# Kernel optimization log

Measured on AMD Instinct MI355X. Metric: run time of the kernel, lower is better.

Reference implementation:

```python
import jax, jax.numpy as jnp
import numpy as np

B, LT, LI, D, H, K = 32, 512, 576, 768, 8, 512


def setup_inputs() -> dict:
    key = jax.random.key(0)
    ks = jax.random.split(key, 10)
    s = 0.02
    return {
        "text_hidden_states": jax.random.normal(ks[0], (B, LT, D), jnp.float32),
        "image_hidden_states": jax.random.normal(ks[1], (B, LI, D), jnp.float32),
        "text_mask": jnp.ones((B, LT), jnp.int32),
        "Wb": jax.random.normal(ks[2], (H, D, D), jnp.float32) * s,   # per-head Linear weights [out,in]
        "Wv": jax.random.normal(ks[3], (K, D), jnp.float32) * s,
        "Wq": jax.random.normal(ks[4], (K, D), jnp.float32) * s,
        "Whv": jax.random.normal(ks[5], (K,), jnp.float32) * s,
        "Whq": jax.random.normal(ks[6], (K,), jnp.float32) * s,
        "Wo": jax.random.normal(ks[7], (D, D * H), jnp.float32) * s,  # output_proj weight [out,in]
        "bo": jnp.zeros((D,), jnp.float32),
    }


def reference(text_hidden_states, image_hidden_states, text_mask, Wb, Wv, Wq, Whv, Whq, Wo, bo):
    text, image = text_hidden_states, image_hidden_states
    # per-head text projection (torch Linear: x @ W.T), batched over heads
    pt = jnp.einsum('bxe,hfe->hbxf', text, Wb)                 # [H,B,LT,D]
    aff = jnp.einsum('hbxe,bye->hbxy', pt, image)              # [H,B,LT,LI]
    wv_v = jnp.einsum('bye,ke->byk', image, Wv)                # [B,LI,K] (head-shared)
    wq_q = jnp.einsum('bxe,ke->bxk', text, Wq)                 # [B,LT,K]
    wqqc = jnp.einsum('bxk,hbxy->hbyk', wq_q, aff)             # [H,B,LI,K]
    wvvc = jnp.einsum('byk,hbxy->hbxk', wv_v, aff)             # [H,B,LT,K]
    h_v = jnp.tanh(wv_v[None] + wqqc)
    h_q = jnp.tanh(wq_q[None] + wvvc)
    att_v = jax.nn.softmax(jnp.einsum('hbyk,k->hby', h_v, Whv), axis=-1)  # over image tokens
    att_q = jax.nn.softmax(jnp.einsum('hbxk,k->hbx', h_q, Whq), axis=-1)  # over text tokens
    ctx_v = jnp.einsum('hby,byd->hbd', att_v, image)
    ctx_q = jnp.einsum('hbx,bxd->hbd', att_q, text)
    head_out = ctx_v + ctx_q                                   # [H,B,D]
    combined = jnp.transpose(head_out, (1, 0, 2)).reshape(text.shape[0], -1)  # [B,H*D]
    return combined @ Wo.T + bo
```

## Files before the change

kernel.cpp:

```cpp
#include <hip/hip_runtime.h>
#include <math.h>

#define B_  32
#define LT_ 512
#define LI_ 576
#define LIP 640
#define D_  768
#define H_  8
#define K_  512
#define NTOK  (LI_ + LT_)
#define CSPLIT 8
#define TPB   (NTOK / CSPLIT)
#define NHEAD ((long)H_ * B_ * D_)

typedef __attribute__((ext_vector_type(4))) short short4v;
typedef __attribute__((ext_vector_type(8))) unsigned short ushort8;
typedef __attribute__((ext_vector_type(8))) _Float16 f16x8;
typedef __attribute__((ext_vector_type(4))) float f32x4;

__device__ __forceinline__ unsigned short f2h(float x) {
  _Float16 h = (_Float16)x;
  return __builtin_bit_cast(unsigned short, h);
}
__device__ __forceinline__ float h2f(unsigned short u) {
  return (float)__builtin_bit_cast(_Float16, u);
}
__device__ __forceinline__ float ftanh(float x) {
  float e = __expf(2.f * x);
  return 1.f - 2.f * __builtin_amdgcn_rcpf(e + 1.f);
}

__device__ __forceinline__ void gl_lds16(const void* g, void* l) {
  __builtin_amdgcn_global_load_lds(
      (const __attribute__((address_space(1))) void*)g,
      (__attribute__((address_space(3))) void*)l, 16, 0, 0);
}

#define EPI_PLAIN 0
#define EPI_T     1
#define EPI_TANH  2
#define EPI_OUT   3

struct Seg {
  const unsigned short *A, *B;
  unsigned short *C, *CT;
  const unsigned short* base;
  const float* wvec;
  float* outv;
  long sA, sB, sC, sCT, sBase;
  int Kd, lda, ldb;
  int gx, gy, nblk, epi, Mlim, valid, ldc, ldt;
};
struct Params { Seg s0, s1, s2; };

__global__ __launch_bounds__(256, 2) void mfma_seg(Params p)
{
  const int orig = blockIdx.x, nwg = gridDim.x;
  const int q8 = nwg >> 3, r8 = nwg & 7;
  const int xcd = orig & 7, idx = orig >> 3;
  const int wg = (xcd < r8 ? xcd * (q8 + 1) : r8 * (q8 + 1) + (xcd - r8) * q8) + idx;

  Seg sg; int local;
  if (wg < p.s0.nblk)                      { sg = p.s0; local = wg; }
  else if (wg < p.s0.nblk + p.s1.nblk)     { sg = p.s1; local = wg - p.s0.nblk; }
  else                                     { sg = p.s2; local = wg - p.s0.nblk - p.s1.nblk; }

  const int bx = local % sg.gx;
  const int tmp2 = local / sg.gx;
  const int by = tmp2 % sg.gy, bz = tmp2 / sg.gy;

  __shared__ unsigned short LDSU[24576];
  unsigned short* As = LDSU;
  unsigned short* Bs = LDSU + 16384;

  const int t = threadIdx.x, lane = t & 63, w = t >> 6;
  const int wr = w >> 1, wc = w & 1;
  const int m0 = bx * 256, n0 = by * 128;
  const int Kd = sg.Kd, lda = sg.lda, ldb = sg.ldb, ldc = sg.ldc;
  const unsigned short* A  = sg.A + (long)bz * sg.sA;
  const unsigned short* Bm = sg.B + (long)bz * sg.sB;

  const int rowb = w * 8 + (lane >> 3);
  const int cswz = ((lane & 7) ^ (rowb & 7)) * 8;
  const bool clampA = (m0 + 256 > sg.Mlim);
  const unsigned short* aSrc = A  + (long)(m0 + rowb) * lda + cswz;
  const unsigned short* bSrc = Bm + (long)(n0 + rowb) * ldb + cswz;
  unsigned short* aDst = As + rowb * 64;
  unsigned short* bDst = Bs + rowb * 64;

  f32x4 acc[8][4];
  #pragma unroll
  for (int i = 0; i < 8; ++i)
    #pragma unroll
    for (int j = 0; j < 4; ++j)
      acc[i][j] = (f32x4){0.f, 0.f, 0.f, 0.f};

  const int rl = lane & 15, g = lane >> 4;

  for (int k0 = 0; k0 < Kd; k0 += 64) {
    __syncthreads();
    if (!clampA) {
      #pragma unroll
      for (int q = 0; q < 8; ++q)
        gl_lds16(aSrc + (long)q * 32 * lda + k0, aDst + q * 2048);
    } else {
      #pragma unroll
      for (int q = 0; q < 8; ++q) {
        int rgl = m0 + q * 32 + rowb;
        if (rgl >= sg.Mlim) rgl = sg.Mlim - 1;
        gl_lds16(A + (long)rgl * lda + cswz + k0, aDst + q * 2048);
      }
    }
    #pragma unroll
    for (int q = 0; q < 4; ++q)
      gl_lds16(bSrc + (long)q * 32 * ldb + k0, bDst + q * 2048);
    __syncthreads();

    #pragma unroll
    for (int h2 = 0; h2 < 2; ++h2) {
      const int slot = (((h2 << 2) | g) ^ (rl & 7)) << 3;
      f16x8 af[8], bf[4];
      #pragma unroll
      for (int i = 0; i < 8; ++i)
        af[i] = *(const f16x8*)&As[(wr * 128 + i * 16 + rl) * 64 + slot];
      #pragma unroll
      for (int j = 0; j < 4; ++j)
        bf[j] = *(const f16x8*)&Bs[(wc * 64 + j * 16 + rl) * 64 + slot];
      #pragma unroll
      for (int i = 0; i < 8; ++i)
        #pragma unroll
        for (int j = 0; j < 4; ++j)
          acc[i][j] = __builtin_amdgcn_mfma_f32_16x16x32_f16(af[i], bf[j], acc[i][j], 0, 0, 0);
    }
  }

  const int rg = lane >> 4;
  if (sg.epi <= EPI_T) {
    unsigned short* C = sg.C + (long)bz * sg.sC;
    #pragma unroll
    for (int i = 0; i < 8; ++i)
      #pragma unroll
      for (int j = 0; j < 4; ++j)
        #pragma unroll
        for (int rr = 0; rr < 4; ++rr) {
          int ml = wr * 128 + i * 16 + rg * 4 + rr;
          int nl = wc * 64 + j * 16 + rl;
          if (m0 + ml < sg.Mlim)
            C[(long)(m0 + ml) * ldc + n0 + nl] = f2h(acc[i][j][rr]);
        }
    if (sg.epi == EPI_T) {
      unsigned short* CT = sg.CT + (long)bz * sg.sCT;
      __syncthreads();
      #pragma unroll
      for (int pp = 0; pp < 2; ++pp) {
        if (wr == pp) {
          #pragma unroll
          for (int i = 0; i < 8; ++i)
            #pragma unroll
            for (int j = 0; j < 4; ++j) {
              int nl = wc * 64 + j * 16 + rl;
              int mh = i * 16 + rg * 4;
              *(short4v*)&LDSU[nl * 136 + mh] = (short4v){
                  (short)f2h(acc[i][j][0]), (short)f2h(acc[i][j][1]),
                  (short)f2h(acc[i][j][2]), (short)f2h(acc[i][j][3])};
            }
        }
        __syncthreads();
        #pragma unroll
        for (int rr = 0; rr < 8; ++rr) {
          int rn = rr * 16 + (t >> 4);
          int m8 = (t & 15) * 8;
          int mg = m0 + pp * 128 + m8;
          if (mg < sg.Mlim)
            *(ushort8*)(CT + (long)(n0 + rn) * sg.ldt + mg) =
                *(const ushort8*)&LDSU[rn * 136 + m8];
        }
        __syncthreads();
      }
    }
  } else if (sg.epi == EPI_TANH) {
    const unsigned short* base = sg.base + (long)bz * sg.sBase;
    float* outp = sg.outv + (long)bz * sg.valid;
    #pragma unroll
    for (int i = 0; i < 8; ++i)
      #pragma unroll
      for (int rr = 0; rr < 4; ++rr) {
        int row = m0 + wr * 128 + i * 16 + rg * 4 + rr;
        if (row < sg.Mlim) {
          float s = 0.f;
          #pragma unroll
          for (int j = 0; j < 4; ++j) {
            int col = n0 + wc * 64 + j * 16 + rl;
            float v = acc[i][j][rr] + h2f(base[(long)row * ldc + col]);
            s += ftanh(v) * sg.wvec[col];
          }
          s += __shfl_xor(s, 1, 64);
          s += __shfl_xor(s, 2, 64);
          s += __shfl_xor(s, 4, 64);
          s += __shfl_xor(s, 8, 64);
          if (rl == 0 && row < sg.valid)
            atomicAdd(&outp[row], s);
        }
      }
  } else {
    float* outp = sg.outv;
    if (wr == 0) {
      #pragma unroll
      for (int i = 0; i < 2; ++i)
        #pragma unroll
        for (int rr = 0; rr < 4; ++rr) {
          int row = i * 16 + rg * 4 + rr;
          #pragma unroll
          for (int j = 0; j < 4; ++j) {
            int col = n0 + wc * 64 + j * 16 + rl;
            atomicAdd(&outp[(long)row * ldc + col], acc[i][j][rr]);
          }
        }
    }
  }
}

struct CSeg { const float* src; unsigned short* dst; long n8; };

__global__ __launch_bounds__(256) void cast_multi(
    CSeg c0, CSeg c1, CSeg c2, CSeg c3, CSeg c4)
{
  long i = (long)blockIdx.x * 256 + threadIdx.x;
  const float* src; unsigned short* dst;
  if      (i < c0.n8)                 { src = c0.src; dst = c0.dst; }
  else if ((i -= c0.n8) < c1.n8)      { src = c1.src; dst = c1.dst; }
  else if ((i -= c1.n8) < c2.n8)      { src = c2.src; dst = c2.dst; }
  else if ((i -= c2.n8) < c3.n8)      { src = c3.src; dst = c3.dst; }
  else if ((i -= c3.n8) < c4.n8)      { src = c4.src; dst = c4.dst; }
  else return;
  float4 v0 = ((const float4*)src)[i * 2];
  float4 v1 = ((const float4*)src)[i * 2 + 1];
  ushort8 o;
  o[0] = f2h(v0.x); o[1] = f2h(v0.y); o[2] = f2h(v0.z); o[3] = f2h(v0.w);
  o[4] = f2h(v1.x); o[5] = f2h(v1.y); o[6] = f2h(v1.z); o[7] = f2h(v1.w);
  *(ushort8*)(dst + i * 8) = o;
}

__global__ __launch_bounds__(256) void cast_pad_image(
    const float* __restrict__ in, unsigned short* __restrict__ out)
{
  long tid = (long)blockIdx.x * 256 + threadIdx.x;
  const long tot = (long)B_ * LIP * (D_ / 8);
  if (tid >= tot) return;
  int e8 = (int)(tid % (D_ / 8));
  long rw = tid / (D_ / 8);
  int y  = (int)(rw % LIP);
  long b = rw / LIP;
  ushort8 o;
  if (y < LI_) {
    const float* p = in + ((b * LI_ + y) * D_ + e8 * 8);
    float4 v0 = *(const float4*)p, v1 = *(const float4*)(p + 4);
    o[0] = f2h(v0.x); o[1] = f2h(v0.y); o[2] = f2h(v0.z); o[3] = f2h(v0.w);
    o[4] = f2h(v1.x); o[5] = f2h(v1.y); o[6] = f2h(v1.z); o[7] = f2h(v1.w);
  } else {
    #pragma unroll
    for (int j = 0; j < 8; ++j) o[j] = 0;
  }
  *(ushort8*)(out + rw * D_ + e8 * 8) = o;
}

__global__ __launch_bounds__(256) void zero_f32(float* __restrict__ p, long n) {
  long i = (long)blockIdx.x * 256 + threadIdx.x;
  if (i < n) p[i] = 0.f;
}

__global__ __launch_bounds__(256) void init_out(
    const float* __restrict__ bo, float* __restrict__ out)
{
  int i = blockIdx.x * 256 + threadIdx.x;
  out[i] = bo[i % D_];
}

__global__ __launch_bounds__(256) void softmax_att(
    const float* __restrict__ lv, const float* __restrict__ lq,
    float* __restrict__ attvG, float* __restrict__ attqG)
{
  const int b = blockIdx.x, h = blockIdx.y;
  const int t = threadIdx.x;
  __shared__ float buf[LI_];
  __shared__ float red[4];

  const float* lvp = lv + ((long)h * B_ + b) * LI_;
  float m = -1e30f;
  for (int i = t; i < LI_; i += 256) m = fmaxf(m, lvp[i]);
  #pragma unroll
  for (int o = 32; o > 0; o >>= 1) m = fmaxf(m, __shfl_down(m, o, 64));
  if ((t & 63) == 0) red[t >> 6] = m;
  __syncthreads();
  m = fmaxf(fmaxf(red[0], red[1]), fmaxf(red[2], red[3]));
  __syncthreads();
  float s = 0.f;
  for (int i = t; i < LI_; i += 256) { float e = __expf(lvp[i] - m); buf[i] = e; s += e; }
  #pragma unroll
  for (int o = 32; o > 0; o >>= 1) s += __shfl_down(s, o, 64);
  if ((t & 63) == 0) red[t >> 6] = s;
  __syncthreads();
  s = red[0] + red[1] + red[2] + red[3];
  {
    float inv = 1.f / s;
    float* op = attvG + ((long)h * B_ + b) * LI_;
    for (int i = t; i < LI_; i += 256) op[i] = buf[i] * inv;
  }
  __syncthreads();

  const float* lqp = lq + ((long)h * B_ + b) * LT_;
  m = -1e30f;
  for (int i = t; i < LT_; i += 256) m = fmaxf(m, lqp[i]);
  #pragma unroll
  for (int o = 32; o > 0; o >>= 1) m = fmaxf(m, __shfl_down(m, o, 64));
  if ((t & 63) == 0) red[t >> 6] = m;
  __syncthreads();
  m = fmaxf(fmaxf(red[0], red[1]), fmaxf(red[2], red[3]));
  __syncthreads();
  s = 0.f;
  for (int i = t; i < LT_; i += 256) { float e = __expf(lqp[i] - m); buf[i] = e; s += e; }
  #pragma unroll
  for (int o = 32; o > 0; o >>= 1) s += __shfl_down(s, o, 64);
  if ((t & 63) == 0) red[t >> 6] = s;
  __syncthreads();
  s = red[0] + red[1] + red[2] + red[3];
  {
    float inv = 1.f / s;
    float* op = attqG + ((long)h * B_ + b) * LT_;
    for (int i = t; i < LT_; i += 256) op[i] = buf[i] * inv;
  }
}

__global__ __launch_bounds__(256) void ctx_part(
    const float* __restrict__ attvG, const float* __restrict__ attqG,
    const unsigned short* __restrict__ text_h,
    float* __restrict__ head_part)
{
  const int b = blockIdx.x, d0 = blockIdx.y * 128, s = blockIdx.z;
  const int t = threadIdx.x, dl = t & 127, g = t >> 7;
  const long IMG_OFF = (long)B_ * LT_ * D_;
  __shared__ float wts[H_][TPB];
  __shared__ long  roff[TPB];
  __shared__ float red[H_][128];
  const int tok0 = s * TPB;
  for (int i = t; i < H_ * TPB; i += 256) {
    int h = i / TPB, j = i % TPB, tok = tok0 + j;
    wts[h][j] = tok < LI_ ? attvG[((long)h * B_ + b) * LI_ + tok]
                          : attqG[((long)h * B_ + b) * LT_ + (tok - LI_)];
  }
  if (t < TPB) {
    int tok = tok0 + t;
    roff[t] = tok < LI_ ? IMG_OFF + ((long)b * LIP + tok) * D_
                        : ((long)b * LT_ + (tok - LI_)) * D_;
  }
  __syncthreads();
  float acc[H_];
  #pragma unroll
  for (int h = 0; h < H_; ++h) acc[h] = 0.f;
  #pragma unroll 4
  for (int j = g; j < TPB; j += 2) {
    float val = h2f(text_h[roff[j] + d0 + dl]);
    #pragma unroll
    for (int h = 0; h < H_; ++h) acc[h] = fmaf(wts[h][j], val, acc[h]);
  }
  if (g == 1) {
    #pragma unroll
    for (int h = 0; h < H_; ++h) red[h][dl] = acc[h];
  }
  __syncthreads();
  if (g == 0) {
    float* hp = head_part + (long)s * NHEAD;
    #pragma unroll
    for (int h = 0; h < H_; ++h)
      hp[((long)h * B_ + b) * D_ + d0 + dl] = acc[h] + red[h][dl];
  }
}

__global__ __launch_bounds__(256) void reduce_head(
    const float* __restrict__ head_part, unsigned short* __restrict__ head16)
{
  long i = (long)blockIdx.x * 256 + threadIdx.x;
  float s = 0.f;
  #pragma unroll
  for (int p = 0; p < CSPLIT; ++p) s += head_part[(long)p * NHEAD + i];
  int d = (int)(i % D_);
  long hb = i / D_;
  int b = (int)(hb % B_), h = (int)(hb / B_);
  head16[(long)b * (H_ * D_) + (long)h * D_ + d] = f2h(s);
}

extern "C" void kernel_launch(void* const* d_in, const int* in_sizes, int n_in,
                              void* d_out, int out_size, void* d_ws, size_t ws_size,
                              hipStream_t stream)
{
  const float* text  = (const float*)d_in[0];
  const float* image = (const float*)d_in[1];
  const float* Wb  = (const float*)d_in[3];
  const float* Wv  = (const float*)d_in[4];
  const float* Wq  = (const float*)d_in[5];
  const float* Whv = (const float*)d_in[6];
  const float* Whq = (const float*)d_in[7];
  const float* Wo  = (const float*)d_in[8];
  const float* bo  = (const float*)d_in[9];
  float* out = (float*)d_out;

  const long N_TEXT = (long)B_ * LT_ * D_;
  const long N_IMGP = (long)B_ * LIP * D_;
  const long N_WV   = (long)K_ * D_;
  const long N_WB   = (long)H_ * D_ * D_;
  const long N_WO   = (long)D_ * H_ * D_;
  const long N_WVV  = (long)B_ * LIP * K_;
  const long N_WQQ  = (long)B_ * LT_ * K_;
  const long N_PT   = (long)B_ * LT_ * D_;
  const long N_AFF  = (long)B_ * LT_ * LIP;
  const long N_LV   = (long)H_ * B_ * LI_;
  const long N_LQ   = (long)H_ * B_ * LT_;
  const long N_H16  = (long)B_ * H_ * D_;

  unsigned short* wsu = (unsigned short*)d_ws;
  long off = 0;
  unsigned short* text_h  = wsu + off; off += N_TEXT;
  unsigned short* image_p = wsu + off; off += N_IMGP;
  unsigned short* Wv_h    = wsu + off; off += N_WV;
  unsigned short* Wq_h    = wsu + off; off += N_WV;
  unsigned short* Wb_h    = wsu + off; off += N_WB;
  unsigned short* Wo_h    = wsu + off; off += N_WO;
  unsigned short* wv_v    = wsu + off; off += N_WVV;
  unsigned short* wq_q    = wsu + off; off += N_WQQ;
  unsigned short* wv_vT   = wsu + off; off += N_WVV;
  unsigned short* wq_qT   = wsu + off; off += N_WQQ;
  unsigned short* pt_h    = wsu + off; off += N_PT;
  unsigned short* aff     = wsu + off; off += N_AFF;
  unsigned short* affT    = wsu + off; off += N_AFF;
  unsigned short* head16  = wsu + off; off += N_H16;
  float* lv        = (float*)(wsu + off);
  float* lq        = lv + N_LV;
  float* attvG     = lq + N_LQ;
  float* attqG     = attvG + N_LV;
  float* head_part = attqG + N_LQ;
  const size_t need = (size_t)off * 2 +
      (size_t)(2 * (N_LV + N_LQ) + CSPLIT * NHEAD) * 4;
  if (ws_size < need) return;

  dim3 blk(256);

  {
    CSeg c0{text, text_h, N_TEXT / 8};
    CSeg c1{Wv,   Wv_h,   N_WV / 8};
    CSeg c2{Wq,   Wq_h,   N_WV / 8};
    CSeg c3{Wb,   Wb_h,   N_WB / 8};
    CSeg c4{Wo,   Wo_h,   N_WO / 8};
    long tot8 = c0.n8 + c1.n8 + c2.n8 + c3.n8 + c4.n8;
    cast_multi<<<(unsigned)((tot8 + 255) / 256), blk, 0, stream>>>(c0, c1, c2, c3, c4);
  }
  cast_pad_image<<<(unsigned)((B_ * LIP * (D_ / 8) + 255) / 256), blk, 0, stream>>>(image, image_p);
  zero_f32<<<(unsigned)((N_LV + N_LQ + 255) / 256), blk, 0, stream>>>(lv, N_LV + N_LQ);
  init_out<<<(unsigned)(B_ * D_ / 256), blk, 0, stream>>>(bo, out);

  Seg zs{};  zs.nblk = 0;

  {
    Seg s0{}; s0.A = image_p; s0.B = Wv_h; s0.C = wv_v; s0.CT = wv_vT;
    s0.sA = (long)LIP * D_; s0.sC = (long)LIP * K_; s0.sCT = (long)K_ * LIP;
    s0.Kd = D_; s0.lda = D_; s0.ldb = D_;
    s0.gx = 3; s0.gy = 4; s0.nblk = 3 * 4 * B_; s0.epi = EPI_T;
    s0.Mlim = LIP; s0.ldc = K_; s0.ldt = LIP;

    Seg s1{}; s1.A = text_h; s1.B = Wq_h; s1.C = wq_q; s1.CT = wq_qT;
    s1.sA = (long)LT_ * D_; s1.sC = (long)LT_ * K_; s1.sCT = (long)K_ * LT_;
    s1.Kd = D_; s1.lda = D_; s1.ldb = D_;
    s1.gx = 2; s1.gy = 4; s1.nblk = 2 * 4 * B_; s1.epi = EPI_T;
    s1.Mlim = LT_; s1.ldc = K_; s1.ldt = LT_;

    Seg s2{}; s2.A = text_h; s2.B = Wb_h; s2.C = pt_h;
    s2.Kd = D_; s2.lda = D_; s2.ldb = D_;
    s2.gx = 64; s2.gy = 6; s2.nblk = 64 * 6; s2.epi = EPI_PLAIN;
    s2.Mlim = B_ * LT_; s2.ldc = D_;

    Params P{s0, s1, s2};
    mfma_seg<<<s0.nblk + s1.nblk + s2.nblk, blk, 0, stream>>>(P);
  }

  for (int h = 0; h < H_; ++h) {
    {
      Seg s0{}; s0.A = pt_h; s0.B = image_p; s0.C = aff; s0.CT = affT;
      s0.sA = (long)LT_ * D_; s0.sB = (long)LIP * D_;
      s0.sC = (long)LT_ * LIP; s0.sCT = (long)LIP * LT_;
      s0.Kd = D_; s0.lda = D_; s0.ldb = D_;
      s0.gx = 2; s0.gy = 5; s0.nblk = 2 * 5 * B_; s0.epi = EPI_T;
      s0.Mlim = LT_; s0.ldc = LIP; s0.ldt = LT_;
      Params P{s0, zs, zs};
      mfma_seg<<<s0.nblk, blk, 0, stream>>>(P);
    }
    {
      Seg s0{}; s0.A = affT; s0.B = wq_qT;
      s0.base = wv_v; s0.wvec = Whv; s0.outv = lv + (long)h * B_ * LI_;
      s0.sA = (long)LIP * LT_; s0.sB = (long)K_ * LT_; s0.sBase = (long)LIP * K_;
      s0.Kd = LT_; s0.lda = LT_; s0.ldb = LT_;
      s0.gx = 3; s0.gy = 4; s0.nblk = 3 * 4 * B_; s0.epi = EPI_TANH;
      s0.Mlim = LIP; s0.valid = LI_; s0.ldc = K_;

      Seg s1{}; s1.A = aff; s1.B = wv_vT;
      s1.base = wq_q; s1.wvec = Whq; s1.outv = lq + (long)h * B_ * LT_;
      s1.sA = (long)LT_ * LIP; s1.sB = (long)K_ * LIP; s1.sBase = (long)LT_ * K_;
      s1.Kd = LIP; s1.lda = LIP; s1.ldb = LIP;
      s1.gx = 2; s1.gy = 4; s1.nblk = 2 * 4 * B_; s1.epi = EPI_TANH;
      s1.Mlim = LT_; s1.valid = LT_; s1.ldc = K_;

      Seg s2 = zs;
      if (h < H_ - 1) {
        s2.A = text_h; s2.B = Wb_h + (long)(h + 1) * D_ * D_; s2.C = pt_h;
        s2.Kd = D_; s2.lda = D_; s2.ldb = D_;
        s2.gx = 64; s2.gy = 6; s2.nblk = 64 * 6; s2.epi = EPI_PLAIN;
        s2.Mlim = B_ * LT_; s2.ldc = D_;
      }
      Params P{s0, s1, s2};
      mfma_seg<<<s0.nblk + s1.nblk + s2.nblk, blk, 0, stream>>>(P);
    }
  }

  softmax_att<<<dim3(B_, H_), blk, 0, stream>>>(lv, lq, attvG, attqG);
  ctx_part<<<dim3(B_, D_ / 128, CSPLIT), blk, 0, stream>>>(attvG, attqG, text_h, head_part);
  reduce_head<<<(unsigned)(NHEAD / 256), blk, 0, stream>>>(head_part, head16);

  {
    Seg s0{}; s0.A = head16; s0.B = Wo_h; s0.outv = out;
    s0.sA = (long)(H_ * D_ / 8); s0.sB = (long)(H_ * D_ / 8);
    s0.Kd = H_ * D_ / 8; s0.lda = H_ * D_; s0.ldb = H_ * D_;
    s0.gx = 1; s0.gy = 6; s0.nblk = 1 * 6 * 8; s0.epi = EPI_OUT;
    s0.Mlim = B_; s0.valid = B_; s0.ldc = D_;
    Params P{s0, zs, zs};
    mfma_seg<<<s0.nblk, blk, 0, stream>>>(P);
  }
}
```

Baseline: 1.037 ms.

## Double-buffer LDS tiles with K-step of 32 in segmented MFMA GEMM

Replaces the single-buffered K=64 LDS tile loop with a double-buffered K=32 pipeline. The next tile is loaded asynchronously into the other LDS buffer while the current tile feeds the MFMAs, and the swizzle pattern is changed to match 32-wide rows. MFMA sections are raised in wave priority with s_setprio. The goal is to hide global-to-LDS load latency behind compute, at the cost of one barrier per smaller K step and twice as many loop iterations.

```diff
diff --git a/kernel.cpp b/kernel.cpp
--- a/kernel.cpp
+++ b/kernel.cpp
@@ -70,8 +70,6 @@
   const int by = tmp2 % sg.gy, bz = tmp2 / sg.gy;
 
   __shared__ unsigned short LDSU[24576];
-  unsigned short* As = LDSU;
-  unsigned short* Bs = LDSU + 16384;
 
   const int t = threadIdx.x, lane = t & 63, w = t >> 6;
   const int wr = w >> 1, wc = w & 1;
@@ -80,13 +78,12 @@
   const unsigned short* A  = sg.A + (long)bz * sg.sA;
   const unsigned short* Bm = sg.B + (long)bz * sg.sB;
 
-  const int rowb = w * 8 + (lane >> 3);
-  const int cswz = ((lane & 7) ^ (rowb & 7)) * 8;
+  const int rowb = w * 16 + (lane >> 2);
+  const int cswz = ((lane & 3) ^ ((rowb >> 1) & 3)) * 8;
   const bool clampA = (m0 + 256 > sg.Mlim);
   const unsigned short* aSrc = A  + (long)(m0 + rowb) * lda + cswz;
   const unsigned short* bSrc = Bm + (long)(n0 + rowb) * ldb + cswz;
-  unsigned short* aDst = As + rowb * 64;
-  unsigned short* bDst = Bs + rowb * 64;
+  const int ldsLane = rowb * 32;
 
   f32x4 acc[8][4];
   #pragma unroll
@@ -96,42 +93,52 @@
       acc[i][j] = (f32x4){0.f, 0.f, 0.f, 0.f};
 
   const int rl = lane & 15, g = lane >> 4;
-
-  for (int k0 = 0; k0 < Kd; k0 += 64) {
-    __syncthreads();
+  const int aslot = (g ^ ((rl >> 1) & 3)) << 3;
+
+  auto stage = [&](int bufi, int k0) {
+    unsigned short* Ab = LDSU + bufi * 12288;
+    unsigned short* Bb = Ab + 8192;
     if (!clampA) {
       #pragma unroll
-      for (int q = 0; q < 8; ++q)
-        gl_lds16(aSrc + (long)q * 32 * lda + k0, aDst + q * 2048);
+      for (int q = 0; q < 4; ++q)
+        gl_lds16(aSrc + (long)q * 64 * lda + k0, Ab + ldsLane + q * 2048);
     } else {
       #pragma unroll
-      for (int q = 0; q < 8; ++q) {
-        int rgl = m0 + q * 32 + rowb;
+      for (int q = 0; q < 4; ++q) {
+        int rgl = m0 + q * 64 + rowb;
         if (rgl >= sg.Mlim) rgl = sg.Mlim - 1;
-        gl_lds16(A + (long)rgl * lda + cswz + k0, aDst + q * 2048);
+        gl_lds16(A + (long)rgl * lda + cswz + k0, Ab + ldsLane + q * 2048);
       }
     }
     #pragma unroll
-    for (int q = 0; q < 4; ++q)
-      gl_lds16(bSrc + (long)q * 32 * ldb + k0, bDst + q * 2048);
+    for (int q = 0; q < 2; ++q)
+      gl_lds16(bSrc + (long)q * 64 * ldb + k0, Bb + ldsLane + q * 2048);
+  };
+
+  const int nt = Kd >> 5;
+  stage(0, 0);
+  __syncthreads();
+  int cur = 0;
+  for (int tt = 0; tt < nt; ++tt) {
+    if (tt + 1 < nt) stage(cur ^ 1, (tt + 1) << 5);
+    const unsigned short* Ab = LDSU + cur * 12288;
+    const unsigned short* Bb = Ab + 8192;
+    f16x8 af[8], bf[4];
+    #pragma unroll
+    for (int i = 0; i < 8; ++i)
+      af[i] = *(const f16x8*)&Ab[(wr * 128 + i * 16 + rl) * 32 + aslot];
+    #pragma unroll
+    for (int j = 0; j < 4; ++j)
+      bf[j] = *(const f16x8*)&Bb[(wc * 64 + j * 16 + rl) * 32 + aslot];
+    __builtin_amdgcn_s_setprio(1);
+    #pragma unroll
+    for (int i = 0; i < 8; ++i)
+      #pragma unroll
+      for (int j = 0; j < 4; ++j)
+        acc[i][j] = __builtin_amdgcn_mfma_f32_16x16x32_f16(af[i], bf[j], acc[i][j], 0, 0, 0);
+    __builtin_amdgcn_s_setprio(0);
     __syncthreads();
-
-    #pragma unroll
-    for (int h2 = 0; h2 < 2; ++h2) {
-      const int slot = (((h2 << 2) | g) ^ (rl & 7)) << 3;
-      f16x8 af[8], bf[4];
-      #pragma unroll
-      for (int i = 0; i < 8; ++i)
-        af[i] = *(const f16x8*)&As[(wr * 128 + i * 16 + rl) * 64 + slot];
-      #pragma unroll
-      for (int j = 0; j < 4; ++j)
-        bf[j] = *(const f16x8*)&Bs[(wc * 64 + j * 16 + rl) * 64 + slot];
-      #pragma unroll
-      for (int i = 0; i < 8; ++i)
-        #pragma unroll
-        for (int j = 0; j < 4; ++j)
-          acc[i][j] = __builtin_amdgcn_mfma_f32_16x16x32_f16(af[i], bf[j], acc[i][j], 0, 0, 0);
-    }
+    cur ^= 1;
   }
 
   const int rg = lane >> 4;
```

New measurement: 1.060 ms. 1.02x slower.
